# Optimization experiments

Hardware: AMD Instinct MI355X
Metric: run time of the kernel (lower is better)

## Reference

```python
import jax, jax.numpy as jnp
import numpy as np

N_SP, N_SPAT = 20000, 10000
E_SS, E_BIP, E_SP = 160000, 320000, 320000
H, C = 4, 64  # GAT heads / per-head channels (hidden_channels=64, concat=False)
EPS = 1e-6


def _gat(xs, xd, row, col, ea, Ws, Wd, a_s, a_d, a_e, We, b, num_dst, heads, ch, self_loops, concat):
    # PyG GATConv with edge_dim: linear -> per-head additive attention -> softmax over incoming edges -> scatter-add
    hs = (xs @ Ws).reshape(-1, heads, ch)          # [Ns,H,C]
    hd = (xd @ Wd).reshape(-1, heads, ch)          # [Nd,H,C]
    al_s = jnp.sum(hs * a_s, -1)                   # [Ns,H]
    al_d = jnp.sum(hd * a_d, -1)                   # [Nd,H]
    if self_loops:
        # add_self_loops with fill_value='mean': loop edge_attr = mean of incoming edge_attr per node
        cnt = jax.ops.segment_sum(jnp.ones((row.shape[0],), ea.dtype), col, num_dst)
        loop_ea = jax.ops.segment_sum(ea, col, num_dst) / jnp.maximum(cnt, 1.0)[:, None]
        loops = jnp.arange(num_dst, dtype=row.dtype)
        row = jnp.concatenate([row, loops])
        col = jnp.concatenate([col, loops])
        ea = jnp.concatenate([ea, loop_ea], 0)
    he = (ea @ We).reshape(-1, heads, ch)          # [E,H,C]
    al = jax.nn.leaky_relu(al_s[row] + al_d[col] + jnp.sum(he * a_e, -1), 0.2)  # [E,H]
    m = jax.ops.segment_max(al, col, num_segments=num_dst)
    ex = jnp.exp(al - m[col])
    den = jax.ops.segment_sum(ex, col, num_segments=num_dst)
    alpha = ex / (den[col] + 1e-16)
    out = jax.ops.segment_sum(hs[row] * alpha[..., None], col, num_segments=num_dst)  # [Nd,H,C]
    out = out.reshape(num_dst, heads * ch) if concat else out.mean(1)
    return out + b


def setup_inputs() -> dict:
    key = jax.random.key(0)
    ks = iter(jax.random.split(key, 64))
    f = lambda shape: jax.random.normal(next(ks), shape, jnp.float32)
    w = lambda shape: f(shape) / np.sqrt(shape[0])
    inp = {}
    inp['species_x_mean'] = f((N_SP, 32))
    inp['species_x_std'] = jax.random.uniform(next(ks), (N_SP, 32), jnp.float32)
    inp['traits_nanmask'] = jax.random.bernoulli(next(ks), 0.4, (N_SP, 32))
    inp['species_x_gen'] = f((N_SP, 64))
    inp['species_x_phylo'] = f((N_SP, 128))
    inp['spatial_x'] = f((N_SPAT, 12))
    inp['spatial_global_data'] = f((N_SPAT, 4))
    ei = lambda e, ns, nd: jnp.stack([jax.random.randint(next(ks), (e,), 0, ns, jnp.int32),
                                      jax.random.randint(next(ks), (e,), 0, nd, jnp.int32)])
    inp['ss_edge_index'] = ei(E_SS, N_SPAT, N_SPAT)
    inp['ss_edge_attr'] = jax.random.uniform(next(ks), (E_SS, 1), jnp.float32)
    inp['bip_edge_index'] = ei(E_BIP, N_SPAT, N_SP)
    inp['bip_edge_attr'] = jax.random.uniform(next(ks), (E_BIP, 1), jnp.float32)
    inp['sp_edge_index'] = ei(E_SP, N_SP, N_SP)
    inp['sp_edge_attr'] = jax.random.uniform(next(ks), (E_SP, 1), jnp.float32)
    # GAT conv params: space_gnn (sg0, sg1), species_gnn (pg0, pg1)
    for nm, din in [('sg0', 16), ('sg1', 64), ('pg0', 128), ('pg1', 64)]:
        inp[nm + '_W'] = w((din, H * C))
        inp[nm + '_as'] = f((H, C)) * 0.1
        inp[nm + '_ad'] = f((H, C)) * 0.1
        inp[nm + '_ae'] = f((H, C)) * 0.1
        inp[nm + '_We'] = w((1, H * C))
        inp[nm + '_b'] = jnp.zeros((C,), jnp.float32)
    # bipartite GATConv: heads=1, concat=True, src dim=hidden=64, dst dim=in_gen+in_phylo=192
    inp['bp_Ws'] = w((64, 64))
    inp['bp_Wd'] = w((192, 64))
    inp['bp_as'] = f((1, 64)) * 0.1
    inp['bp_ad'] = f((1, 64)) * 0.1
    inp['bp_ae'] = f((1, 64)) * 0.1
    inp['bp_We'] = w((1, 64))
    inp['bp_b'] = jnp.zeros((64,), jnp.float32)
    inp['sl_W'] = w((288, 64))
    inp['sl_b'] = jnp.zeros((64,), jnp.float32)
    inp['fc_W'] = w((64, 64))
    inp['fc_b'] = jnp.zeros((64,), jnp.float32)
    return inp


def reference(species_x_mean, species_x_std, traits_nanmask, species_x_gen, species_x_phylo,
              spatial_x, spatial_global_data, ss_edge_index, ss_edge_attr, bip_edge_index,
              bip_edge_attr, sp_edge_index, sp_edge_attr,
              sg0_W, sg0_as, sg0_ad, sg0_ae, sg0_We, sg0_b,
              sg1_W, sg1_as, sg1_ad, sg1_ae, sg1_We, sg1_b,
              pg0_W, pg0_as, pg0_ad, pg0_ae, pg0_We, pg0_b,
              pg1_W, pg1_as, pg1_ad, pg1_ae, pg1_We, pg1_b,
              bp_Ws, bp_Wd, bp_as, bp_ad, bp_ae, bp_We, bp_b,
              sl_W, sl_b, fc_W, fc_b):
    # inference path: no trait masking -> visibility = observed mask
    vis = (~traits_nanmask).astype(jnp.float32)
    sp_in = jnp.concatenate([species_x_mean, species_x_std, vis, species_x_gen, species_x_phylo], 1)
    sp_in = jax.nn.relu(sp_in @ sl_W + sl_b)                      # [N_SP,64]
    # spatial GNN (2 GATConv layers, heads=4, concat=False, self loops)
    h = jnp.concatenate([spatial_x, spatial_global_data], 1)      # [N_SPAT,16]
    r, c = ss_edge_index[0], ss_edge_index[1]
    h = jax.nn.relu(_gat(h, h, r, c, ss_edge_attr, sg0_W, sg0_W, sg0_as, sg0_ad, sg0_ae, sg0_We, sg0_b, N_SPAT, H, C, True, False))
    h = jax.nn.relu(_gat(h, h, r, c, ss_edge_attr, sg1_W, sg1_W, sg1_as, sg1_ad, sg1_ae, sg1_We, sg1_b, N_SPAT, H, C, True, False))
    # bipartite spatial->species GATConv (heads=1, concat=True, no self loops)
    part = jnp.concatenate([species_x_gen, species_x_phylo], 1)   # [N_SP,192]
    br, bc = bip_edge_index[0], bip_edge_index[1]
    sts = jax.nn.relu(_gat(h, part, br, bc, bip_edge_attr, bp_Ws, bp_Wd, bp_as, bp_ad, bp_ae, bp_We, bp_b, N_SP, 1, 64, False, True))
    # species GNN (2 GATConv layers)
    x = jnp.concatenate([sts, sp_in], 1)                          # [N_SP,128]
    pr, pc = sp_edge_index[0], sp_edge_index[1]
    x = jax.nn.relu(_gat(x, x, pr, pc, sp_edge_attr, pg0_W, pg0_W, pg0_as, pg0_ad, pg0_ae, pg0_We, pg0_b, N_SP, H, C, True, False))
    x = jax.nn.relu(_gat(x, x, pr, pc, sp_edge_attr, pg1_W, pg1_W, pg1_as, pg1_ad, pg1_ae, pg1_We, pg1_b, N_SP, H, C, True, False))
    ms = x @ fc_W + fc_b                                          # [N_SP, 2*out]
    mean, log_std = jnp.split(ms, 2, axis=-1)
    std = jax.nn.softplus(log_std) + EPS
    return mean, std
```

## Files before the change

### kernel.cpp

```cpp
#include <hip/hip_runtime.h>
#include <hip/hip_bf16.h>

#define NSP   20000
#define NSPAT 10000
#define ESS   160000
#define EBIP  320000
#define ESP   320000

static inline int cdiv_host(long a, long b) { return (int)((a + b - 1) / b); }

__device__ __forceinline__ float wave_red_sum(float p) {
#pragma unroll
  for (int m = 32; m >= 1; m >>= 1) p += __shfl_xor(p, m, 64);
  return p;
}
__device__ __forceinline__ float bf2f(unsigned short u) {
  return __uint_as_float(((unsigned int)u) << 16);
}
__device__ __forceinline__ unsigned short f2bf(float f) {
  unsigned int u = __float_as_uint(f);
  unsigned int r = (u + 0x7FFF + ((u >> 16) & 1)) >> 16;
  return (unsigned short)r;
}

// ... 220 lines not shown
  }

  float4 bv = make_float4(0.f, 0.f, 0.f, 0.f);
  float4 asv = make_float4(0.f, 0.f, 0.f, 0.f);
  float4 adv = make_float4(0.f, 0.f, 0.f, 0.f);
  if (J.bias) bv = *(const float4*)(J.bias + c0);
  if (J.a_s) asv = *(const float4*)(J.a_s + c0);
  if (J.a_d) adv = *(const float4*)(J.a_d + c0);

#pragma unroll
  for (int r = 0; r < 2; ++r) {
    long m = row0 + rg * 2 + r;
    bool ok = m < J.M;
    float v0 = acc[r][0] + bv.x, v1 = acc[r][1] + bv.y;
    float v2 = acc[r][2] + bv.z, v3 = acc[r][3] + bv.w;
    if (J.mode == 1) {
      if (ok)
        *(float4*)(J.Y + m * 64 + c0) = make_float4(
            fmaxf(v0, 0.f), fmaxf(v1, 0.f), fmaxf(v2, 0.f), fmaxf(v3, 0.f));
    } else if (J.mode == 2) {
      if (ok) {
        if (c0 < 32) {
          *(float4*)(J.Y + m * 32 + c0) = make_float4(v0, v1, v2, v3);
        } else {
          float4 o;
          o.x = fmaxf(v0, 0.f) + log1pf(__expf(-fabsf(v0))) + 1e-6f;
          o.y = fmaxf(v1, 0.f) + log1pf(__expf(-fabsf(v1))) + 1e-6f;
          o.z = fmaxf(v2, 0.f) + log1pf(__expf(-fabsf(v2))) + 1e-6f;
          o.w = fmaxf(v3, 0.f) + log1pf(__expf(-fabsf(v3))) + 1e-6f;
          *(float4*)(J.Y2 + m * 32 + (c0 - 32)) = o;
        }
      }
    } else if (ok && J.Y) {
      *(float4*)(J.Y + m * 64 + c0) = make_float4(v0, v1, v2, v3);
    }
    if (J.a_s) {
      float s = acc[r][0] * asv.x + acc[r][1] * asv.y + acc[r][2] * asv.z + acc[r][3] * asv.w;
      s += __shfl_xor(s, 1); s += __shfl_xor(s, 2);
      s += __shfl_xor(s, 4); s += __shfl_xor(s, 8);
      if (ok && cg == 0) J.al_s[m] = s;
    }
    if (J.a_d) {
      float s = acc[r][0] * adv.x + acc[r][1] * adv.y + acc[r][2] * adv.z + acc[r][3] * adv.w;
      s += __shfl_xor(s, 1); s += __shfl_xor(s, 2);
      s += __shfl_xor(s, 4); s += __shfl_xor(s, 8);
      if (ok && cg == 0) J.al_d[m] = s;
    }
  }
}

__global__ __launch_bounds__(256) void proj64x2l_kernel(PJob j0, PJob j1,
                                                        int nb0, int nb1,
                                                        LeafArgs la) {
  __shared__ float wl[32 * 64];
  __shared__ float xl[32 * 36];
  int b = blockIdx.x, t = threadIdx.x;
  if (b < nb0) {
    proj64_body(j0, b, wl, xl);
  } else if (b < nb0 + nb1) {
    proj64_body(j1, b - nb0, wl, xl);
  } else {
    int i = (b - nb0 - nb1) * 256 + t;
    if (i >= NSPAT + NSP) return;
    const int* ptr; const float* cea; float* lea; int d;
    if (i < NSPAT) { ptr = la.ss_ptr; cea = la.ss_cea; lea = la.ss_lea; d = i; }
    else { ptr = la.pp_ptr; cea = la.pp_cea; lea = la.pp_lea; d = i - NSPAT; }
    int e0 = ptr[d], e1 = ptr[d + 1];
    float s = 0.f;
    for (int e = e0; e < e1; ++e) s += cea[e];
    lea[d] = s / (float)max(e1 - e0, 1);
  }
}

__global__ __launch_bounds__(256) void proj_kernel(
    XSrc xsrc, int M, int K,
    const float* __restrict__ W,
    const float* __restrict__ a_s, const float* __restrict__ a_d,
    float* __restrict__ al_s, float* __restrict__ al_d,
    unsigned short* __restrict__ Y) {
  constexpr int KC = 32;
  constexpr int RPT = 8;
  constexpr int BR = 32;
  constexpr int KCP = 36;
  constexpr int H = 4;
  __shared__ float wl[KC * 256];
  __shared__ float xl[BR * KCP];

  int t = threadIdx.x;
  int cg = t & 63, rg = t >> 6;
  int c0 = cg * 4;
  long row0 = (long)blockIdx.x * BR;

  float acc[RPT][4];
#pragma unroll
  for (int r = 0; r < RPT; ++r)
#pragma unroll
    for (int j = 0; j < 4; ++j) acc[r][j] = 0.f;

  for (int k0 = 0; k0 < K; k0 += KC) {
    int kc = min(KC, K - k0);
    int seg = 0; int base = 0;
    while (k0 >= base + xsrc.w[seg]) { base += xsrc.w[seg]; ++seg; }
    const float* Xp = xsrc.p[seg];
    int stride = xsrc.w[seg];
    int kloc = k0 - base;

    __syncthreads();
    {
      const float4* wsrc = (const float4*)(W + (long)k0 * 256);
      float4* wdst = (float4*)wl;
      for (int i = t; i < (kc * 256) >> 2; i += 256) wdst[i] = wsrc[i];
    }
    for (int i = t; i < BR * 8; i += 256) {
      int r = i >> 3, kq = (i & 7) * 4;
      if (kq < kc) {
        long rr = row0 + r; if (rr >= M) rr = M - 1;
        float4 v = *(const float4*)(Xp + rr * stride + kloc + kq);
        *(float4*)(xl + r * KCP + kq) = v;
      }
    }
    __syncthreads();

    for (int kg = 0; kg < kc; kg += 4) {
      float4 w0 = *(const float4*)(wl + (kg + 0) * 256 + c0);
      float4 w1 = *(const float4*)(wl + (kg + 1) * 256 + c0);
      float4 w2 = *(const float4*)(wl + (kg + 2) * 256 + c0);
      float4 w3 = *(const float4*)(wl + (kg + 3) * 256 + c0);
      float4 xv[RPT];
#pragma unroll
      for (int r = 0; r < RPT; ++r)
        xv[r] = *(const float4*)(xl + (rg * RPT + r) * KCP + kg);
#pragma unroll
      for (int r = 0; r < RPT; ++r) {
        acc[r][0] = fmaf(xv[r].x, w0.x, acc[r][0]);
        acc[r][1] = fmaf(xv[r].x, w0.y, acc[r][1]);
        acc[r][2] = fmaf(xv[r].x, w0.z, acc[r][2]);
        acc[r][3] = fmaf(xv[r].x, w0.w, acc[r][3]);
        acc[r][0] = fmaf(xv[r].y, w1.x, acc[r][0]);
        acc[r][1] = fmaf(xv[r].y, w1.y, acc[r][1]);
        acc[r][2] = fmaf(xv[r].y, w1.z, acc[r][2]);
        acc[r][3] = fmaf(xv[r].y, w1.w, acc[r][3]);
        acc[r][0] = fmaf(xv[r].z, w2.x, acc[r][0]);
        acc[r][1] = fmaf(xv[r].z, w2.y, acc[r][1]);
        acc[r][2] = fmaf(xv[r].z, w2.z, acc[r][2]);
        acc[r][3] = fmaf(xv[r].z, w2.w, acc[r][3]);
        acc[r][0] = fmaf(xv[r].w, w3.x, acc[r][0]);
        acc[r][1] = fmaf(xv[r].w, w3.y, acc[r][1]);
        acc[r][2] = fmaf(xv[r].w, w3.z, acc[r][2]);
        acc[r][3] = fmaf(xv[r].w, w3.w, acc[r][3]);
      }
    }
  }

  float4 asv = *(const float4*)(a_s + c0);
  float4 adv = *(const float4*)(a_d + c0);

#pragma unroll
  for (int r = 0; r < RPT; ++r) {
    long m = row0 + (long)rg * RPT + r;
    bool ok = m < M;
    if (ok) {
      ushort4 o;
      o.x = f2bf(acc[r][0]); o.y = f2bf(acc[r][1]);
      o.z = f2bf(acc[r][2]); o.w = f2bf(acc[r][3]);
      *(ushort4*)(Y + m * 256 + c0) = o;
    }
    float s = acc[r][0] * asv.x + acc[r][1] * asv.y + acc[r][2] * asv.z + acc[r][3] * asv.w;
    s += __shfl_xor(s, 1); s += __shfl_xor(s, 2);
    s += __shfl_xor(s, 4); s += __shfl_xor(s, 8);
    if (ok && (cg & 15) == 0) al_s[m * H + (c0 >> 6)] = s;
    float d = acc[r][0] * adv.x + acc[r][1] * adv.y + acc[r][2] * adv.z + acc[r][3] * adv.w;
    d += __shfl_xor(d, 1); d += __shfl_xor(d, 2);
    d += __shfl_xor(d, 4); d += __shfl_xor(d, 8);
    if (ok && (cg & 15) == 0) al_d[m * H + (c0 >> 6)] = d;
  }
}

__device__ __forceinline__ void fma4_bf(float4& a, float al, ushort4 u) {
  a.x = fmaf(al, bf2f(u.x), a.x); a.y = fmaf(al, bf2f(u.y), a.y);
  a.z = fmaf(al, bf2f(u.z), a.z); a.w = fmaf(al, bf2f(u.w), a.w);
}
__device__ __forceinline__ void scale4(float4& a, float s) {
  a.x *= s; a.y *= s; a.z *= s; a.w *= s;
}

template <bool SELFLOOP>
__global__ __launch_bounds__(256) void gat4_fused(
    int Nd, const int* __restrict__ dptr, const int* __restrict__ csr_src,
    const float* __restrict__ csr_ea, const float* __restrict__ al_s,
    const float* __restrict__ al_d, const float* __restrict__ dote,
    const float* __restrict__ loop_ea, const unsigned short* __restrict__ hs,
    const float* __restrict__ bias, float* __restrict__ out) {
  int wave = threadIdx.x >> 6, lane = threadIdx.x & 63;
  int n = blockIdx.x * 4 + wave;
  if (n >= Nd) return;
  int h = lane >> 4;
  float ald = al_d[(long)n * 4 + h];
  float de = dote[h];
  int e0 = dptr[n], e1 = dptr[n + 1];
  float m0 = -INFINITY, d0 = 0.f;
  float4 a0 = make_float4(0.f, 0.f, 0.f, 0.f);
  if (SELFLOOP) {
    float l = al_s[(long)n * 4 + h] + ald + loop_ea[n] * de;
    l = (l > 0.f) ? l : 0.2f * l;
    m0 = l; d0 = 1.f;
    ushort4 u = *(const ushort4*)(hs + (long)n * 256 + lane * 4);
    a0.x = bf2f(u.x); a0.y = bf2f(u.y); a0.z = bf2f(u.z); a0.w = bf2f(u.w);
  }
  float m1 = -INFINITY, d1 = 0.f;
  float4 a1 = make_float4(0.f, 0.f, 0.f, 0.f);
  int e = e0;
  for (; e + 2 <= e1; e += 2) {
    int s0 = csr_src[e], s1 = csr_src[e + 1];
    float l0 = al_s[(long)s0 * 4 + h] + ald + csr_ea[e] * de;
    float l1 = al_s[(long)s1 * 4 + h] + ald + csr_ea[e + 1] * de;
    l0 = (l0 > 0.f) ? l0 : 0.2f * l0;
    l1 = (l1 > 0.f) ? l1 : 0.2f * l1;
    ushort4 u0 = *(const ushort4*)(hs + (long)s0 * 256 + lane * 4);
    ushort4 u1 = *(const ushort4*)(hs + (long)s1 * 256 + lane * 4);
    if (l0 > m0) { float sc = __expf(m0 - l0); d0 *= sc; scale4(a0, sc); m0 = l0; }
    float ex0 = __expf(l0 - m0);
    d0 += ex0;
    fma4_bf(a0, ex0, u0);
    if (l1 > m1) { float sc = __expf(m1 - l1); d1 *= sc; scale4(a1, sc); m1 = l1; }
    float ex1 = __expf(l1 - m1);
    d1 += ex1;
    fma4_bf(a1, ex1, u1);
  }
  if (e < e1) {
    int s0 = csr_src[e];
    float l0 = al_s[(long)s0 * 4 + h] + ald + csr_ea[e] * de;
    l0 = (l0 > 0.f) ? l0 : 0.2f * l0;
    ushort4 u0 = *(const ushort4*)(hs + (long)s0 * 256 + lane * 4);
    if (l0 > m0) { float sc = __expf(m0 - l0); d0 *= sc; scale4(a0, sc); m0 = l0; }
    float ex0 = __expf(l0 - m0);
    d0 += ex0;
    fma4_bf(a0, ex0, u0);
  }
  if (m1 != -INFINITY) {
    float M = fmaxf(m0, m1);
    float sA = (m0 == -INFINITY) ? 0.f : __expf(m0 - M);
    float sB = __expf(m1 - M);
    d0 = d0 * sA + d1 * sB;
    a0.x = a0.x * sA + a1.x * sB; a0.y = a0.y * sA + a1.y * sB;
    a0.z = a0.z * sA + a1.z * sB; a0.w = a0.w * sA + a1.w * sB;
  }
  float inv = 1.f / (d0 + 1e-16f);
  scale4(a0, inv);
  a0.x += __shfl_xor(a0.x, 16); a0.y += __shfl_xor(a0.y, 16);
  a0.z += __shfl_xor(a0.z, 16); a0.w += __shfl_xor(a0.w, 16);
  a0.x += __shfl_xor(a0.x, 32); a0.y += __shfl_xor(a0.y, 32);
  a0.z += __shfl_xor(a0.z, 32); a0.w += __shfl_xor(a0.w, 32);
  if (lane < 16) {
    float4 b = *(const float4*)(bias + lane * 4);
    float4 o;
    o.x = fmaxf(a0.x * 0.25f + b.x, 0.f);
    o.y = fmaxf(a0.y * 0.25f + b.y, 0.f);
    o.z = fmaxf(a0.z * 0.25f + b.z, 0.f);
    o.w = fmaxf(a0.w * 0.25f + b.w, 0.f);
    *(float4*)(out + (long)n * 64 + lane * 4) = o;
  }
}

__global__ __launch_bounds__(256) void gat1_fused(
    int Nd, const int* __restrict__ dptr, const int* __restrict__ csr_src,
    const float* __restrict__ csr_ea, const float* __restrict__ al_s,
    const float* __restrict__ al_d, const float* __restrict__ dote,
    const float* __restrict__ hs, const float* __restrict__ bias,
    float* __restrict__ out) {
  int wave = threadIdx.x >> 6, lane = threadIdx.x & 63;
  int n = blockIdx.x * 4 + wave;
  if (n >= Nd) return;
  float ald = al_d[n];
  float de = dote[0];
  int e0 = dptr[n], e1 = dptr[n + 1];
  float m0 = -INFINITY, d0 = 0.f, acc0 = 0.f;
  float m1 = -INFINITY, d1 = 0.f, acc1 = 0.f;
  int e = e0;
  for (; e + 2 <= e1; e += 2) {
    int s0 = csr_src[e], s1 = csr_src[e + 1];
    float l0 = al_s[s0] + ald + csr_ea[e] * de;
    float l1 = al_s[s1] + ald + csr_ea[e + 1] * de;
    l0 = (l0 > 0.f) ? l0 : 0.2f * l0;
    l1 = (l1 > 0.f) ? l1 : 0.2f * l1;
    float h0 = hs[(long)s0 * 64 + lane];
    float h1 = hs[(long)s1 * 64 + lane];
    if (l0 > m0) { float sc = __expf(m0 - l0); d0 *= sc; acc0 *= sc; m0 = l0; }
    float ex0 = __expf(l0 - m0);
    d0 += ex0; acc0 = fmaf(ex0, h0, acc0);
    if (l1 > m1) { float sc = __expf(m1 - l1); d1 *= sc; acc1 *= sc; m1 = l1; }
    float ex1 = __expf(l1 - m1);
    d1 += ex1; acc1 = fmaf(ex1, h1, acc1);
  }
  if (e < e1) {
    int s0 = csr_src[e];
    float l0 = al_s[s0] + ald + csr_ea[e] * de;
    l0 = (l0 > 0.f) ? l0 : 0.2f * l0;
    float h0 = hs[(long)s0 * 64 + lane];
    if (l0 > m0) { float sc = __expf(m0 - l0); d0 *= sc; acc0 *= sc; m0 = l0; }
    float ex0 = __expf(l0 - m0);
    d0 += ex0; acc0 = fmaf(ex0, h0, acc0);
  }
  if (m1 != -INFINITY) {
    float M = fmaxf(m0, m1);
    float sA = (m0 == -INFINITY) ? 0.f : __expf(m0 - M);
    float sB = __expf(m1 - M);
    d0 = d0 * sA + d1 * sB;
    acc0 = acc0 * sA + acc1 * sB;
  }
  float o = acc0 / (d0 + 1e-16f);
  out[(long)n * 64 + lane] = fmaxf(o + bias[lane], 0.f);
}

extern "C" void kernel_launch(void* const* d_in, const int* in_sizes, int n_in,
                              void* d_out, int out_size, void* d_ws, size_t ws_size,
                              hipStream_t stream) {
  const float* sp_mean = (const float*)d_in[0];
  const float* sp_std  = (const float*)d_in[1];
  const void*  nanmask = d_in[2];
  const float* sp_gen  = (const float*)d_in[3];
  const float* sp_phy  = (const float*)d_in[4];
  const float* spat_x  = (const float*)d_in[5];
  const float* spat_g  = (const float*)d_in[6];
  const int*   ss_ei   = (const int*)d_in[7];
  const float* ss_ea   = (const float*)d_in[8];
  const int*   bip_ei  = (const int*)d_in[9];
  const float* bip_ea  = (const float*)d_in[10];
  const int*   sp_ei   = (const int*)d_in[11];
  const float* sp_ea   = (const float*)d_in[12];
  const float* sg0_W = (const float*)d_in[13]; const float* sg0_as = (const float*)d_in[14];
  const float* sg0_ad = (const float*)d_in[15]; const float* sg0_ae = (const float*)d_in[16];
  const float* sg0_We = (const float*)d_in[17]; const float* sg0_b = (const float*)d_in[18];
  const float* sg1_W = (const float*)d_in[19]; const float* sg1_as = (const float*)d_in[20];
  const float* sg1_ad = (const float*)d_in[21]; const float* sg1_ae = (const float*)d_in[22];
  const float* sg1_We = (const float*)d_in[23]; const float* sg1_b = (const float*)d_in[24];
  const float* pg0_W = (const float*)d_in[25]; const float* pg0_as = (const float*)d_in[26];
  const float* pg0_ad = (const float*)d_in[27]; const float* pg0_ae = (const float*)d_in[28];
  const float* pg0_We = (const float*)d_in[29]; const float* pg0_b = (const float*)d_in[30];
  const float* pg1_W = (const float*)d_in[31]; const float* pg1_as = (const float*)d_in[32];
  const float* pg1_ad = (const float*)d_in[33]; const float* pg1_ae = (const float*)d_in[34];
  const float* pg1_We = (const float*)d_in[35]; const float* pg1_b = (const float*)d_in[36];
  const float* bp_Ws = (const float*)d_in[37]; const float* bp_Wd = (const float*)d_in[38];
  const float* bp_as = (const float*)d_in[39]; const float* bp_ad = (const float*)d_in[40];
  const float* bp_ae = (const float*)d_in[41]; const float* bp_We = (const float*)d_in[42];
  const float* bp_b  = (const float*)d_in[43];
  const float* sl_W  = (const float*)d_in[44]; const float* sl_b  = (const float*)d_in[45];
  const float* fc_W  = (const float*)d_in[46]; const float* fc_b  = (const float*)d_in[47];

  char* wsb = (char*)d_ws;
  size_t off = 0;
  auto A = [&](size_t nbytes) -> void* {
    void* p = wsb + off;
    off += (nbytes + 255) & ~(size_t)255;
    return p;
  };
  int* ss_cp = (int*)A((size_t)8 * NSPAT * 4);
  int* bp_cp = (int*)A((size_t)8 * NSP * 4);
  int* pp_cp = (int*)A((size_t)8 * NSP * 4);
  size_t zbytes = off;
  int*   ss_cnt = (int*)A((NSPAT + 1) * 4);
  int*   bp_cnt = (int*)A((NSP + 1) * 4);
  int*   pp_cnt = (int*)A((NSP + 1) * 4);
  int*   flag  = (int*)A(4);
  float* dotes = (float*)A(5 * 4 * sizeof(float));
  float* alS   = (float*)A((size_t)NSP * 4 * 4);
  float* alD   = (float*)A((size_t)NSP * 4 * 4);
  float* alSb  = (float*)A((size_t)NSPAT * 4);
  float* alDb  = (float*)A((size_t)NSP * 4);
  float* spc96 = (float*)A((size_t)NSP * 96 * 4);
  float* sp_in = (float*)A((size_t)NSP * 64 * 4);
  float* h0    = (float*)A((size_t)NSPAT * 16 * 4);
  float* h_a   = (float*)A((size_t)NSPAT * 64 * 4);
  float* h_b   = (float*)A((size_t)NSPAT * 64 * 4);
  float* HS    = (float*)A((size_t)NSP * 256 * 4);
  float* sts   = (float*)A((size_t)NSP * 64 * 4);
  float* x1    = (float*)A((size_t)NSP * 64 * 4);
  int*   ss_ptr = (int*)A((NSPAT + 1) * 4);
  int*   ss_src = (int*)A((size_t)ESS * 4);
  float* ss_cea = (float*)A((size_t)ESS * 4);
  int*   ss_rnk = (int*)A((size_t)ESS * 4);
  float* ss_lea = (float*)A((size_t)NSPAT * 4);
  int*   bp_ptr = (int*)A((NSP + 1) * 4);
  int*   bp_src = (int*)A((size_t)EBIP * 4);
  float* bp_cea = (float*)A((size_t)EBIP * 4);
  int*   bp_rnk = (int*)A((size_t)EBIP * 4);
  int*   pp_ptr = (int*)A((NSP + 1) * 4);
  int*   pp_src = (int*)A((size_t)ESP * 4);
  float* pp_cea = (float*)A((size_t)ESP * 4);
  int*   pp_rnk = (int*)A((size_t)ESP * 4);
  float* pp_lea = (float*)A((size_t)NSP * 4);
  (void)ws_size; (void)in_sizes; (void)n_in; (void)out_size;

  const int TB = 256;
  hipMemsetAsync(wsb, 0, zbytes, stream);

  count3_kernel<<<cdiv_host(ESS + EBIP + ESP, TB) + 1, TB, 0, stream>>>(
      ss_ei + ESS, ESS, ss_cp, ss_rnk, NSPAT,
      bip_ei + EBIP, EBIP, bp_cp, bp_rnk, NSP,
      sp_ei + ESP, ESP, pp_cp, pp_rnk, NSP,
      (const unsigned int*)nanmask, flag);
  merge3_kernel<<<cdiv_host(NSPAT + NSP + NSP, TB), TB, 0, stream>>>(
      ss_cp, ss_cnt, NSPAT, bp_cp, bp_cnt, NSP, pp_cp, pp_cnt, NSP);
  scan3_kernel<<<3, 1024, 0, stream>>>(ss_cnt, NSPAT, ss_ptr, bp_cnt, NSP, bp_ptr, pp_cnt, NSP, pp_ptr);

  {
    DoteArgs da{};
    da.We[0] = sg0_We; da.ae[0] = sg0_ae;
    da.We[1] = sg1_We; da.ae[1] = sg1_ae;
    da.We[2] = bp_We;  da.ae[2] = bp_ae;
    da.We[3] = pg0_We; da.ae[3] = pg0_ae;
    da.We[4] = pg1_We; da.ae[4] = pg1_ae;
    da.dotes = dotes;
    PrepArgs pa{ sp_mean, sp_std, nanmask, flag, spat_x, spat_g, spc96, h0 };
    int nb = cdiv_host(ESS + EBIP + ESP, TB) + 5 +
             cdiv_host((long)NSP * 96 + (long)NSPAT * 16, TB);
    scatter3x_kernel<<<nb, TB, 0, stream>>>(
        ss_ei, ss_ei + ESS, ss_ea, ESS, ss_ptr, ss_cp, ss_rnk, NSPAT, ss_src, ss_cea,
        bip_ei, bip_ei + EBIP, bip_ea, EBIP, bp_ptr, bp_cp, bp_rnk, NSP, bp_src, bp_cea,
        sp_ei, sp_ei + ESP, sp_ea, ESP, pp_ptr, pp_cp, pp_rnk, NSP, pp_src, pp_cea,
        da, pa);
  }

  {
    PJob j0{}; j0.xs.p[0] = spc96; j0.xs.w[0] = 96; j0.xs.p[1] = sp_gen; j0.xs.w[1] = 64;
    j0.xs.p[2] = sp_phy; j0.xs.w[2] = 128; j0.xs.n = 3;
    j0.M = NSP; j0.K = 288; j0.W = sl_W; j0.bias = sl_b; j0.mode = 1; j0.Y = sp_in;
    PJob j1{}; j1.xs.p[0] = sp_gen; j1.xs.w[0] = 64; j1.xs.p[1] = sp_phy; j1.xs.w[1] = 128;
    j1.xs.n = 2;
    j1.M = NSP; j1.K = 192; j1.W = bp_Wd; j1.mode = 0; j1.a_d = bp_ad; j1.al_d = alDb;
    LeafArgs la{ ss_ptr, ss_cea, ss_lea, pp_ptr, pp_cea, pp_lea };
    int nb0 = cdiv_host(NSP, 32), nb1 = cdiv_host(NSP, 32);
    int nbl = cdiv_host(NSPAT + NSP, TB);
    proj64x2l_kernel<<<nb0 + nb1 + nbl, TB, 0, stream>>>(j0, j1, nb0, nb1, la);
  }

  {
    XSrc xs{}; xs.p[0] = h0; xs.w[0] = 16; xs.n = 1;
    proj_kernel<<<cdiv_host(NSPAT, 32), TB, 0, stream>>>(xs, NSPAT, 16, sg0_W,
        sg0_as, sg0_ad, alS, alD, (unsigned short*)HS);
  }
  gat4_fused<true><<<cdiv_host(NSPAT, 4), TB, 0, stream>>>(
      NSPAT, ss_ptr, ss_src, ss_cea, alS, alD, dotes + 0, ss_lea,
      (const unsigned short*)HS, sg0_b, h_a);
  {
    XSrc xs{}; xs.p[0] = h_a; xs.w[0] = 64; xs.n = 1;
    proj_kernel<<<cdiv_host(NSPAT, 32), TB, 0, stream>>>(xs, NSPAT, 64, sg1_W,
        sg1_as, sg1_ad, alS, alD, (unsigned short*)HS);
  }
  gat4_fused<true><<<cdiv_host(NSPAT, 4), TB, 0, stream>>>(
      NSPAT, ss_ptr, ss_src, ss_cea, alS, alD, dotes + 4, ss_lea,
      (const unsigned short*)HS, sg1_b, h_b);

  {
    PJob j0{}; j0.xs.p[0] = h_b; j0.xs.w[0] = 64; j0.xs.n = 1;
    j0.M = NSPAT; j0.K = 64; j0.W = bp_Ws; j0.mode = 0;
    j0.a_s = bp_as; j0.al_s = alSb; j0.Y = h_a;
    LeafArgs la{ ss_ptr, ss_cea, ss_lea, pp_ptr, pp_cea, pp_lea };
    int nb0 = cdiv_host(NSPAT, 32);
    proj64x2l_kernel<<<nb0, TB, 0, stream>>>(j0, j0, nb0, 0, la);
  }
  gat1_fused<<<cdiv_host(NSP, 4), TB, 0, stream>>>(
      NSP, bp_ptr, bp_src, bp_cea, alSb, alDb, dotes + 8, h_a, bp_b, sts);

  {
    XSrc xs{}; xs.p[0] = sts; xs.w[0] = 64; xs.p[1] = sp_in; xs.w[1] = 64; xs.n = 2;
    proj_kernel<<<cdiv_host(NSP, 32), TB, 0, stream>>>(xs, NSP, 128, pg0_W,
        pg0_as, pg0_ad, alS, alD, (unsigned short*)HS);
  }
  gat4_fused<true><<<cdiv_host(NSP, 4), TB, 0, stream>>>(
      NSP, pp_ptr, pp_src, pp_cea, alS, alD, dotes + 12, pp_lea,
      (const unsigned short*)HS, pg0_b, x1);
  {
    XSrc xs{}; xs.p[0] = x1; xs.w[0] = 64; xs.n = 1;
    proj_kernel<<<cdiv_host(NSP, 32), TB, 0, stream>>>(xs, NSP, 64, pg1_W,
        pg1_as, pg1_ad, alS, alD, (unsigned short*)HS);
  }
  gat4_fused<true><<<cdiv_host(NSP, 4), TB, 0, stream>>>(
      NSP, pp_ptr, pp_src, pp_cea, alS, alD, dotes + 16, pp_lea,
      (const unsigned short*)HS, pg1_b, sts);

  {
    PJob j0{}; j0.xs.p[0] = sts; j0.xs.w[0] = 64; j0.xs.n = 1;
    j0.M = NSP; j0.K = 64; j0.W = fc_W; j0.bias = fc_b; j0.mode = 2;
    j0.Y = (float*)d_out; j0.Y2 = (float*)d_out + (long)NSP * 32;
    LeafArgs la{ ss_ptr, ss_cea, ss_lea, pp_ptr, pp_cea, pp_lea };
    int nb0 = cdiv_host(NSP, 32);
    proj64x2l_kernel<<<nb0, TB, 0, stream>>>(j0, j0, nb0, 0, la);
  }
}
```

Measured before the change: 497.0 us.

## Fuse GAT aggregation with the following projection through shared-memory tiles

Each GAT aggregation kernel now writes its 32-node output tile into shared memory, and the next layer's projection (256-wide or 64-wide, including the final FC/softplus head) runs in the same block from that tile. This removes the global-memory round trip of intermediate node features and cuts the launch count. Attention and feature buffers are double-buffered (A/B) so a layer can read the previous projection while writing the next. In exchange, each block now processes 8 nodes per wave sequentially, which gives fewer waves and less latency hiding in the gather phase, and it uses more LDS per block.

```diff
diff --git a/kernel.cpp b/kernel.cpp
--- a/kernel.cpp
+++ b/kernel.cpp
@@ -326,7 +326,6 @@
   constexpr int RPT = 8;
   constexpr int BR = 32;
   constexpr int KCP = 36;
-  constexpr int H = 4;
   __shared__ float wl[KC * 256];
   __shared__ float xl[BR * KCP];
 
@@ -412,11 +411,11 @@
     float s = acc[r][0] * asv.x + acc[r][1] * asv.y + acc[r][2] * asv.z + acc[r][3] * asv.w;
     s += __shfl_xor(s, 1); s += __shfl_xor(s, 2);
     s += __shfl_xor(s, 4); s += __shfl_xor(s, 8);
-    if (ok && (cg & 15) == 0) al_s[m * H + (c0 >> 6)] = s;
+    if (ok && (cg & 15) == 0) al_s[m * 4 + (c0 >> 6)] = s;
     float d = acc[r][0] * adv.x + acc[r][1] * adv.y + acc[r][2] * adv.z + acc[r][3] * adv.w;
     d += __shfl_xor(d, 1); d += __shfl_xor(d, 2);
     d += __shfl_xor(d, 4); d += __shfl_xor(d, 8);
-    if (ok && (cg & 15) == 0) al_d[m * H + (c0 >> 6)] = d;
+    if (ok && (cg & 15) == 0) al_d[m * 4 + (c0 >> 6)] = d;
   }
 }
 
@@ -428,132 +427,348 @@
   a.x *= s; a.y *= s; a.z *= s; a.w *= s;
 }
 
-template <bool SELFLOOP>
-__global__ __launch_bounds__(256) void gat4_fused(
-    int Nd, const int* __restrict__ dptr, const int* __restrict__ csr_src,
-    const float* __restrict__ csr_ea, const float* __restrict__ al_s,
-    const float* __restrict__ al_d, const float* __restrict__ dote,
-    const float* __restrict__ loop_ea, const unsigned short* __restrict__ hs,
-    const float* __restrict__ bias, float* __restrict__ out) {
+struct G4A {
+  int Nd;
+  const int* dptr; const int* src; const float* cea;
+  const float* al_s; const float* al_d; const float* dote;
+  const float* lea; const unsigned short* hs; const float* bias;
+};
+struct G1A {
+  int Nd;
+  const int* dptr; const int* src; const float* cea;
+  const float* al_s; const float* al_d; const float* dote;
+  const float* hs; const float* bias;
+};
+struct PF256 {
+  int M, K;
+  const float* W; const float* xg;
+  const float* a_s; const float* a_d;
+  float* al_s; float* al_d;
+  unsigned short* Y;
+};
+struct PF64 {
+  int M;
+  const float* W; const float* bias; int mode;
+  const float* a_s; float* al_s;
+  float* Y; float* Y2;
+};
+
+__device__ void gat4_phase(const G4A& g, int b, float* hbuf) {
   int wave = threadIdx.x >> 6, lane = threadIdx.x & 63;
-  int n = blockIdx.x * 4 + wave;
-  if (n >= Nd) return;
   int h = lane >> 4;
-  float ald = al_d[(long)n * 4 + h];
-  float de = dote[h];
-  int e0 = dptr[n], e1 = dptr[n + 1];
-  float m0 = -INFINITY, d0 = 0.f;
-  float4 a0 = make_float4(0.f, 0.f, 0.f, 0.f);
-  if (SELFLOOP) {
-    float l = al_s[(long)n * 4 + h] + ald + loop_ea[n] * de;
+  float de = g.dote[h];
+  for (int i = 0; i < 8; ++i) {
+    int ln = wave * 8 + i;
+    int n = b * 32 + ln;
+    if (n >= g.Nd) continue;
+    float ald = g.al_d[(long)n * 4 + h];
+    int e0 = g.dptr[n], e1 = g.dptr[n + 1];
+    float l = g.al_s[(long)n * 4 + h] + ald + g.lea[n] * de;
     l = (l > 0.f) ? l : 0.2f * l;
-    m0 = l; d0 = 1.f;
-    ushort4 u = *(const ushort4*)(hs + (long)n * 256 + lane * 4);
-    a0.x = bf2f(u.x); a0.y = bf2f(u.y); a0.z = bf2f(u.z); a0.w = bf2f(u.w);
-  }
-  float m1 = -INFINITY, d1 = 0.f;
-  float4 a1 = make_float4(0.f, 0.f, 0.f, 0.f);
-  int e = e0;
-  for (; e + 2 <= e1; e += 2) {
-    int s0 = csr_src[e], s1 = csr_src[e + 1];
-    float l0 = al_s[(long)s0 * 4 + h] + ald + csr_ea[e] * de;
-    float l1 = al_s[(long)s1 * 4 + h] + ald + csr_ea[e + 1] * de;
-    l0 = (l0 > 0.f) ? l0 : 0.2f * l0;
-    l1 = (l1 > 0.f) ? l1 : 0.2f * l1;
-    ushort4 u0 = *(const ushort4*)(hs + (long)s0 * 256 + lane * 4);
-    ushort4 u1 = *(const ushort4*)(hs + (long)s1 * 256 + lane * 4);
-    if (l0 > m0) { float sc = __expf(m0 - l0); d0 *= sc; scale4(a0, sc); m0 = l0; }
-    float ex0 = __expf(l0 - m0);
-    d0 += ex0;
-    fma4_bf(a0, ex0, u0);
-    if (l1 > m1) { float sc = __expf(m1 - l1); d1 *= sc; scale4(a1, sc); m1 = l1; }
-    float ex1 = __expf(l1 - m1);
-    d1 += ex1;
-    fma4_bf(a1, ex1, u1);
-  }
-  if (e < e1) {
-    int s0 = csr_src[e];
-    float l0 = al_s[(long)s0 * 4 + h] + ald + csr_ea[e] * de;
-    l0 = (l0 > 0.f) ? l0 : 0.2f * l0;
-    ushort4 u0 = *(const ushort4*)(hs + (long)s0 * 256 + lane * 4);
-    if (l0 > m0) { float sc = __expf(m0 - l0); d0 *= sc; scale4(a0, sc); m0 = l0; }
-    float ex0 = __expf(l0 - m0);
-    d0 += ex0;
-    fma4_bf(a0, ex0, u0);
-  }
-  if (m1 != -INFINITY) {
-    float M = fmaxf(m0, m1);
-    float sA = (m0 == -INFINITY) ? 0.f : __expf(m0 - M);
-    float sB = __expf(m1 - M);
-    d0 = d0 * sA + d1 * sB;
-    a0.x = a0.x * sA + a1.x * sB; a0.y = a0.y * sA + a1.y * sB;
-    a0.z = a0.z * sA + a1.z * sB; a0.w = a0.w * sA + a1.w * sB;
-  }
-  float inv = 1.f / (d0 + 1e-16f);
-  scale4(a0, inv);
-  a0.x += __shfl_xor(a0.x, 16); a0.y += __shfl_xor(a0.y, 16);
-  a0.z += __shfl_xor(a0.z, 16); a0.w += __shfl_xor(a0.w, 16);
-  a0.x += __shfl_xor(a0.x, 32); a0.y += __shfl_xor(a0.y, 32);
-  a0.z += __shfl_xor(a0.z, 32); a0.w += __shfl_xor(a0.w, 32);
-  if (lane < 16) {
-    float4 b = *(const float4*)(bias + lane * 4);
-    float4 o;
-    o.x = fmaxf(a0.x * 0.25f + b.x, 0.f);
-    o.y = fmaxf(a0.y * 0.25f + b.y, 0.f);
-    o.z = fmaxf(a0.z * 0.25f + b.z, 0.f);
-    o.w = fmaxf(a0.w * 0.25f + b.w, 0.f);
-    *(float4*)(out + (long)n * 64 + lane * 4) = o;
-  }
-}
-
-__global__ __launch_bounds__(256) void gat1_fused(
-    int Nd, const int* __restrict__ dptr, const int* __restrict__ csr_src,
-    const float* __restrict__ csr_ea, const float* __restrict__ al_s,
-    const float* __restrict__ al_d, const float* __restrict__ dote,
-    const float* __restrict__ hs, const float* __restrict__ bias,
-    float* __restrict__ out) {
+    float m0 = l, d0 = 1.f;
+    float4 a0;
+    {
+      ushort4 u = *(const ushort4*)(g.hs + (long)n * 256 + lane * 4);
+      a0.x = bf2f(u.x); a0.y = bf2f(u.y); a0.z = bf2f(u.z); a0.w = bf2f(u.w);
+    }
+    float m1 = -INFINITY, d1 = 0.f;
+    float4 a1 = make_float4(0.f, 0.f, 0.f, 0.f);
+    int e = e0;
+    for (; e + 2 <= e1; e += 2) {
+      int s0 = g.src[e], s1 = g.src[e + 1];
+      float l0 = g.al_s[(long)s0 * 4 + h] + ald + g.cea[e] * de;
+      float l1 = g.al_s[(long)s1 * 4 + h] + ald + g.cea[e + 1] * de;
+      l0 = (l0 > 0.f) ? l0 : 0.2f * l0;
+      l1 = (l1 > 0.f) ? l1 : 0.2f * l1;
+      ushort4 u0 = *(const ushort4*)(g.hs + (long)s0 * 256 + lane * 4);
+      ushort4 u1 = *(const ushort4*)(g.hs + (long)s1 * 256 + lane * 4);
+      if (l0 > m0) { float sc = __expf(m0 - l0); d0 *= sc; scale4(a0, sc); m0 = l0; }
+      float ex0 = __expf(l0 - m0);
+      d0 += ex0;
+      fma4_bf(a0, ex0, u0);
+      if (l1 > m1) { float sc = __expf(m1 - l1); d1 *= sc; scale4(a1, sc); m1 = l1; }
+      float ex1 = __expf(l1 - m1);
+      d1 += ex1;
+      fma4_bf(a1, ex1, u1);
+    }
+    if (e < e1) {
+      int s0 = g.src[e];
+      float l0 = g.al_s[(long)s0 * 4 + h] + ald + g.cea[e] * de;
+      l0 = (l0 > 0.f) ? l0 : 0.2f * l0;
+      ushort4 u0 = *(const ushort4*)(g.hs + (long)s0 * 256 + lane * 4);
+      if (l0 > m0) { float sc = __expf(m0 - l0); d0 *= sc; scale4(a0, sc); m0 = l0; }
+      float ex0 = __expf(l0 - m0);
+      d0 += ex0;
+      fma4_bf(a0, ex0, u0);
+    }
+    if (m1 != -INFINITY) {
+      float M = fmaxf(m0, m1);
+      float sA = __expf(m0 - M);
+      float sB = __expf(m1 - M);
+      d0 = d0 * sA + d1 * sB;
+      a0.x = a0.x * sA + a1.x * sB; a0.y = a0.y * sA + a1.y * sB;
+      a0.z = a0.z * sA + a1.z * sB; a0.w = a0.w * sA + a1.w * sB;
+    }
+    float inv = 1.f / (d0 + 1e-16f);
+    scale4(a0, inv);
+    a0.x += __shfl_xor(a0.x, 16); a0.y += __shfl_xor(a0.y, 16);
+    a0.z += __shfl_xor(a0.z, 16); a0.w += __shfl_xor(a0.w, 16);
+    a0.x += __shfl_xor(a0.x, 32); a0.y += __shfl_xor(a0.y, 32);
+    a0.z += __shfl_xor(a0.z, 32); a0.w += __shfl_xor(a0.w, 32);
+    if (lane < 16) {
+      float4 bv = *(const float4*)(g.bias + lane * 4);
+      float4 o;
+      o.x = fmaxf(a0.x * 0.25f + bv.x, 0.f);
+      o.y = fmaxf(a0.y * 0.25f + bv.y, 0.f);
+      o.z = fmaxf(a0.z * 0.25f + bv.z, 0.f);
+      o.w = fmaxf(a0.w * 0.25f + bv.w, 0.f);
+      *(float4*)(hbuf + ln * 64 + lane * 4) = o;
+    }
+  }
+}
+
+__device__ void gat1_phase(const G1A& g, int b, float* hbuf) {
   int wave = threadIdx.x >> 6, lane = threadIdx.x & 63;
-  int n = blockIdx.x * 4 + wave;
-  if (n >= Nd) return;
-  float ald = al_d[n];
-  float de = dote[0];
-  int e0 = dptr[n], e1 = dptr[n + 1];
-  float m0 = -INFINITY, d0 = 0.f, acc0 = 0.f;
-  float m1 = -INFINITY, d1 = 0.f, acc1 = 0.f;
-  int e = e0;
-  for (; e + 2 <= e1; e += 2) {
-    int s0 = csr_src[e], s1 = csr_src[e + 1];
-    float l0 = al_s[s0] + ald + csr_ea[e] * de;
-    float l1 = al_s[s1] + ald + csr_ea[e + 1] * de;
-    l0 = (l0 > 0.f) ? l0 : 0.2f * l0;
-    l1 = (l1 > 0.f) ? l1 : 0.2f * l1;
-    float h0 = hs[(long)s0 * 64 + lane];
-    float h1 = hs[(long)s1 * 64 + lane];
-    if (l0 > m0) { float sc = __expf(m0 - l0); d0 *= sc; acc0 *= sc; m0 = l0; }
-    float ex0 = __expf(l0 - m0);
-    d0 += ex0; acc0 = fmaf(ex0, h0, acc0);
-    if (l1 > m1) { float sc = __expf(m1 - l1); d1 *= sc; acc1 *= sc; m1 = l1; }
-    float ex1 = __expf(l1 - m1);
-    d1 += ex1; acc1 = fmaf(ex1, h1, acc1);
-  }
-  if (e < e1) {
-    int s0 = csr_src[e];
-    float l0 = al_s[s0] + ald + csr_ea[e] * de;
-    l0 = (l0 > 0.f) ? l0 : 0.2f * l0;
-    float h0 = hs[(long)s0 * 64 + lane];
-    if (l0 > m0) { float sc = __expf(m0 - l0); d0 *= sc; acc0 *= sc; m0 = l0; }
-    float ex0 = __expf(l0 - m0);
-    d0 += ex0; acc0 = fmaf(ex0, h0, acc0);
-  }
-  if (m1 != -INFINITY) {
-    float M = fmaxf(m0, m1);
-    float sA = (m0 == -INFINITY) ? 0.f : __expf(m0 - M);
-    float sB = __expf(m1 - M);
-    d0 = d0 * sA + d1 * sB;
-    acc0 = acc0 * sA + acc1 * sB;
-  }
-  float o = acc0 / (d0 + 1e-16f);
-  out[(long)n * 64 + lane] = fmaxf(o + bias[lane], 0.f);
+  float de = g.dote[0];
+  for (int i = 0; i < 8; ++i) {
+    int ln = wave * 8 + i;
+    int n = b * 32 + ln;
+    if (n >= g.Nd) continue;
+    float ald = g.al_d[n];
+    int e0 = g.dptr[n], e1 = g.dptr[n + 1];
+    float m0 = -INFINITY, d0 = 0.f, acc0 = 0.f;
+    float m1 = -INFINITY, d1 = 0.f, acc1 = 0.f;
+    int e = e0;
+    for (; e + 2 <= e1; e += 2) {
+      int s0 = g.src[e], s1 = g.src[e + 1];
+      float l0 = g.al_s[s0] + ald + g.cea[e] * de;
+      float l1 = g.al_s[s1] + ald + g.cea[e + 1] * de;
+      l0 = (l0 > 0.f) ? l0 : 0.2f * l0;
+      l1 = (l1 > 0.f) ? l1 : 0.2f * l1;
+      float h0 = g.hs[(long)s0 * 64 + lane];
+      float h1 = g.hs[(long)s1 * 64 + lane];
+      if (l0 > m0) { float sc = __expf(m0 - l0); d0 *= sc; acc0 *= sc; m0 = l0; }
+      float ex0 = __expf(l0 - m0);
+      d0 += ex0; acc0 = fmaf(ex0, h0, acc0);
+      if (l1 > m1) { float sc = __expf(m1 - l1); d1 *= sc; acc1 *= sc; m1 = l1; }
+      float ex1 = __expf(l1 - m1);
+      d1 += ex1; acc1 = fmaf(ex1, h1, acc1);
+    }
+    if (e < e1) {
+      int s0 = g.src[e];
+      float l0 = g.al_s[s0] + ald + g.cea[e] * de;
+      l0 = (l0 > 0.f) ? l0 : 0.2f * l0;
+      float h0 = g.hs[(long)s0 * 64 + lane];
+      if (l0 > m0) { float sc = __expf(m0 - l0); d0 *= sc; acc0 *= sc; m0 = l0; }
+      float ex0 = __expf(l0 - m0);
+      d0 += ex0; acc0 = fmaf(ex0, h0, acc0);
+    }
+    if (m1 != -INFINITY) {
+      float M = fmaxf(m0, m1);
+      float sA = (m0 == -INFINITY) ? 0.f : __expf(m0 - M);
+      float sB = __expf(m1 - M);
+      d0 = d0 * sA + d1 * sB;
+      acc0 = acc0 * sA + acc1 * sB;
+    }
+    float o = acc0 / (d0 + 1e-16f);
+    hbuf[ln * 64 + lane] = fmaxf(o + g.bias[lane], 0.f);
+  }
+}
+
+__device__ void proj256_fused(const PF256& p, int b, const float* hbuf,
+                              float* wl, float* xl) {
+  constexpr int KC = 32, RPT = 8, KCP = 36;
+  int t = threadIdx.x;
+  int cg = t & 63, rg = t >> 6;
+  int c0 = cg * 4;
+  long row0 = (long)b * 32;
+
+  float acc[RPT][4];
+#pragma unroll
+  for (int r = 0; r < RPT; ++r)
+#pragma unroll
+    for (int j = 0; j < 4; ++j) acc[r][j] = 0.f;
+
+  for (int k0 = 0; k0 < p.K; k0 += KC) {
+    bool fromLds = (k0 < 64);
+    __syncthreads();
+    {
+      const float4* wsrc = (const float4*)(p.W + (long)k0 * 256);
+      float4* wdst = (float4*)wl;
+      for (int i = t; i < (KC * 256) >> 2; i += 256) wdst[i] = wsrc[i];
+    }
+    if (!fromLds) {
+      int r = t >> 3, kq = (t & 7) * 4;
+      long rr = row0 + r; if (rr >= p.M) rr = p.M - 1;
+      float4 v = *(const float4*)(p.xg + rr * 64 + (k0 - 64) + kq);
+      *(float4*)(xl + r * KCP + kq) = v;
+    }
+    __syncthreads();
+
+    for (int kg = 0; kg < KC; kg += 4) {
+      float4 w0 = *(const float4*)(wl + (kg + 0) * 256 + c0);
+      float4 w1 = *(const float4*)(wl + (kg + 1) * 256 + c0);
+      float4 w2 = *(const float4*)(wl + (kg + 2) * 256 + c0);
+      float4 w3 = *(const float4*)(wl + (kg + 3) * 256 + c0);
+      float4 xv[RPT];
+#pragma unroll
+      for (int r = 0; r < RPT; ++r)
+        xv[r] = fromLds ? *(const float4*)(hbuf + (rg * RPT + r) * 64 + k0 + kg)
+                        : *(const float4*)(xl + (rg * RPT + r) * KCP + kg);
+#pragma unroll
+      for (int r = 0; r < RPT; ++r) {
+        acc[r][0] = fmaf(xv[r].x, w0.x, acc[r][0]);
+        acc[r][1] = fmaf(xv[r].x, w0.y, acc[r][1]);
+        acc[r][2] = fmaf(xv[r].x, w0.z, acc[r][2]);
+        acc[r][3] = fmaf(xv[r].x, w0.w, acc[r][3]);
+        acc[r][0] = fmaf(xv[r].y, w1.x, acc[r][0]);
+        acc[r][1] = fmaf(xv[r].y, w1.y, acc[r][1]);
+        acc[r][2] = fmaf(xv[r].y, w1.z, acc[r][2]);
+        acc[r][3] = fmaf(xv[r].y, w1.w, acc[r][3]);
+        acc[r][0] = fmaf(xv[r].z, w2.x, acc[r][0]);
+        acc[r][1] = fmaf(xv[r].z, w2.y, acc[r][1]);
+        acc[r][2] = fmaf(xv[r].z, w2.z, acc[r][2]);
+        acc[r][3] = fmaf(xv[r].z, w2.w, acc[r][3]);
+        acc[r][0] = fmaf(xv[r].w, w3.x, acc[r][0]);
+        acc[r][1] = fmaf(xv[r].w, w3.y, acc[r][1]);
+        acc[r][2] = fmaf(xv[r].w, w3.z, acc[r][2]);
+        acc[r][3] = fmaf(xv[r].w, w3.w, acc[r][3]);
+      }
+    }
+  }
+
+  float4 asv = *(const float4*)(p.a_s + c0);
+  float4 adv = *(const float4*)(p.a_d + c0);
+#pragma unroll
+  for (int r = 0; r < RPT; ++r) {
+    long m = row0 + (long)rg * RPT + r;
+    bool ok = m < p.M;
+    if (ok) {
+      ushort4 o;
+      o.x = f2bf(acc[r][0]); o.y = f2bf(acc[r][1]);
+      o.z = f2bf(acc[r][2]); o.w = f2bf(acc[r][3]);
+      *(ushort4*)(p.Y + m * 256 + c0) = o;
+    }
+    float s = acc[r][0] * asv.x + acc[r][1] * asv.y + acc[r][2] * asv.z + acc[r][3] * asv.w;
+    s += __shfl_xor(s, 1); s += __shfl_xor(s, 2);
+    s += __shfl_xor(s, 4); s += __shfl_xor(s, 8);
+    if (ok && (cg & 15) == 0) p.al_s[m * 4 + (c0 >> 6)] = s;
+    float d = acc[r][0] * adv.x + acc[r][1] * adv.y + acc[r][2] * adv.z + acc[r][3] * adv.w;
+    d += __shfl_xor(d, 1); d += __shfl_xor(d, 2);
+    d += __shfl_xor(d, 4); d += __shfl_xor(d, 8);
+    if (ok && (cg & 15) == 0) p.al_d[m * 4 + (c0 >> 6)] = d;
+  }
+}
+
+__device__ void proj64_fused(const PF64& p, int b, const float* hbuf, float* wl) {
+  int t = threadIdx.x;
+  int cg = t & 15, rg = t >> 4;
+  int c0 = cg * 4;
+  long row0 = (long)b * 32;
+
+  float acc[2][4];
+#pragma unroll
+  for (int r = 0; r < 2; ++r)
+#pragma unroll
+    for (int j = 0; j < 4; ++j) acc[r][j] = 0.f;
+
+  for (int k0 = 0; k0 < 64; k0 += 32) {
+    __syncthreads();
+    {
+      const float4* ws = (const float4*)(p.W + (long)k0 * 64);
+      float4* wd = (float4*)wl;
+      wd[t] = ws[t];
+      wd[t + 256] = ws[t + 256];
+    }
+    __syncthreads();
+    for (int kg = 0; kg < 32; kg += 4) {
+      float4 w0 = *(const float4*)(wl + (kg + 0) * 64 + c0);
+      float4 w1 = *(const float4*)(wl + (kg + 1) * 64 + c0);
+      float4 w2 = *(const float4*)(wl + (kg + 2) * 64 + c0);
+      float4 w3 = *(const float4*)(wl + (kg + 3) * 64 + c0);
+#pragma unroll
+      for (int r = 0; r < 2; ++r) {
+        float4 xv = *(const float4*)(hbuf + (rg * 2 + r) * 64 + k0 + kg);
+        acc[r][0] = fmaf(xv.x, w0.x, acc[r][0]);
+        acc[r][1] = fmaf(xv.x, w0.y, acc[r][1]);
+        acc[r][2] = fmaf(xv.x, w0.z, acc[r][2]);
+        acc[r][3] = fmaf(xv.x, w0.w, acc[r][3]);
+        acc[r][0] = fmaf(xv.y, w1.x, acc[r][0]);
+        acc[r][1] = fmaf(xv.y, w1.y, acc[r][1]);
+        acc[r][2] = fmaf(xv.y, w1.z, acc[r][2]);
+        acc[r][3] = fmaf(xv.y, w1.w, acc[r][3]);
+        acc[r][0] = fmaf(xv.z, w2.x, acc[r][0]);
+        acc[r][1] = fmaf(xv.z, w2.y, acc[r][1]);
+        acc[r][2] = fmaf(xv.z, w2.z, acc[r][2]);
+        acc[r][3] = fmaf(xv.z, w2.w, acc[r][3]);
+        acc[r][0] = fmaf(xv.w, w3.x, acc[r][0]);
+        acc[r][1] = fmaf(xv.w, w3.y, acc[r][1]);
+        acc[r][2] = fmaf(xv.w, w3.z, acc[r][2]);
+        acc[r][3] = fmaf(xv.w, w3.w, acc[r][3]);
+      }
+    }
+  }
+
+  float4 bv = make_float4(0.f, 0.f, 0.f, 0.f);
+  float4 asv = make_float4(0.f, 0.f, 0.f, 0.f);
+  if (p.bias) bv = *(const float4*)(p.bias + c0);
+  if (p.a_s) asv = *(const float4*)(p.a_s + c0);
+
+#pragma unroll
+  for (int r = 0; r < 2; ++r) {
+    long m = row0 + rg * 2 + r;
+    bool ok = m < p.M;
+    float v0 = acc[r][0] + bv.x, v1 = acc[r][1] + bv.y;
+    float v2 = acc[r][2] + bv.z, v3 = acc[r][3] + bv.w;
+    if (p.mode == 2) {
+      if (ok) {
+        if (c0 < 32) {
+          *(float4*)(p.Y + m * 32 + c0) = make_float4(v0, v1, v2, v3);
+        } else {
+          float4 o;
+          o.x = fmaxf(v0, 0.f) + log1pf(__expf(-fabsf(v0))) + 1e-6f;
+          o.y = fmaxf(v1, 0.f) + log1pf(__expf(-fabsf(v1))) + 1e-6f;
+          o.z = fmaxf(v2, 0.f) + log1pf(__expf(-fabsf(v2))) + 1e-6f;
+          o.w = fmaxf(v3, 0.f) + log1pf(__expf(-fabsf(v3))) + 1e-6f;
+          *(float4*)(p.Y2 + m * 32 + (c0 - 32)) = o;
+        }
+      }
+    } else if (ok && p.Y) {
+      *(float4*)(p.Y + m * 64 + c0) = make_float4(v0, v1, v2, v3);
+    }
+    if (p.a_s) {
+      float s = acc[r][0] * asv.x + acc[r][1] * asv.y + acc[r][2] * asv.z + acc[r][3] * asv.w;
+      s += __shfl_xor(s, 1); s += __shfl_xor(s, 2);
+      s += __shfl_xor(s, 4); s += __shfl_xor(s, 8);
+      if (ok && cg == 0) p.al_s[m] = s;
+    }
+  }
+}
+
+__global__ __launch_bounds__(256) void g4p256_kernel(G4A g, PF256 p) {
+  __shared__ __align__(16) float wl[32 * 256];
+  __shared__ __align__(16) float xl[32 * 36];
+  __shared__ __align__(16) float hbuf[32 * 64];
+  gat4_phase(g, blockIdx.x, hbuf);
+  __syncthreads();
+  proj256_fused(p, blockIdx.x, hbuf, wl, xl);
+}
+
+__global__ __launch_bounds__(256) void g1p256_kernel(G1A g, PF256 p) {
+  __shared__ __align__(16) float wl[32 * 256];
+  __shared__ __align__(16) float xl[32 * 36];
+  __shared__ __align__(16) float hbuf[32 * 64];
+  gat1_phase(g, blockIdx.x, hbuf);
+  __syncthreads();
+  proj256_fused(p, blockIdx.x, hbuf, wl, xl);
+}
+
+__global__ __launch_bounds__(256) void g4p64_kernel(G4A g, PF64 p) {
+  __shared__ __align__(16) float wl[32 * 64];
+  __shared__ __align__(16) float hbuf[32 * 64];
+  gat4_phase(g, blockIdx.x, hbuf);
+  __syncthreads();
+  proj64_fused(p, blockIdx.x, hbuf, wl);
 }
 
 extern "C" void kernel_launch(void* const* d_in, const int* in_sizes, int n_in,
@@ -607,18 +822,18 @@
   int*   pp_cnt = (int*)A((NSP + 1) * 4);
   int*   flag  = (int*)A(4);
   float* dotes = (float*)A(5 * 4 * sizeof(float));
-  float* alS   = (float*)A((size_t)NSP * 4 * 4);
-  float* alD   = (float*)A((size_t)NSP * 4 * 4);
+  float* alS_A = (float*)A((size_t)NSP * 4 * 4);
+  float* alD_A = (float*)A((size_t)NSP * 4 * 4);
+  float* alS_B = (float*)A((size_t)NSP * 4 * 4);
+  float* alD_B = (float*)A((size_t)NSP * 4 * 4);
   float* alSb  = (float*)A((size_t)NSPAT * 4);
   float* alDb  = (float*)A((size_t)NSP * 4);
   float* spc96 = (float*)A((size_t)NSP * 96 * 4);
   float* sp_in = (float*)A((size_t)NSP * 64 * 4);
   float* h0    = (float*)A((size_t)NSPAT * 16 * 4);
-  float* h_a   = (float*)A((size_t)NSPAT * 64 * 4);
-  float* h_b   = (float*)A((size_t)NSPAT * 64 * 4);
-  float* HS    = (float*)A((size_t)NSP * 256 * 4);
-  float* sts   = (float*)A((size_t)NSP * 64 * 4);
-  float* x1    = (float*)A((size_t)NSP * 64 * 4);
+  float* h_src = (float*)A((size_t)NSPAT * 64 * 4);
+  unsigned short* HS_A = (unsigned short*)A((size_t)NSP * 256 * 2);
+  unsigned short* HS_B = (unsigned short*)A((size_t)NSP * 256 * 2);
   int*   ss_ptr = (int*)A((NSPAT + 1) * 4);
   int*   ss_src = (int*)A((size_t)ESS * 4);
   float* ss_cea = (float*)A((size_t)ESS * 4);
@@ -681,54 +896,37 @@
   {
     XSrc xs{}; xs.p[0] = h0; xs.w[0] = 16; xs.n = 1;
     proj_kernel<<<cdiv_host(NSPAT, 32), TB, 0, stream>>>(xs, NSPAT, 16, sg0_W,
-        sg0_as, sg0_ad, alS, alD, (unsigned short*)HS);
-  }
-  gat4_fused<true><<<cdiv_host(NSPAT, 4), TB, 0, stream>>>(
-      NSPAT, ss_ptr, ss_src, ss_cea, alS, alD, dotes + 0, ss_lea,
-      (const unsigned short*)HS, sg0_b, h_a);
+        sg0_as, sg0_ad, alS_A, alD_A, HS_A);
+  }
+
   {
-    XSrc xs{}; xs.p[0] = h_a; xs.w[0] = 64; xs.n = 1;
-    proj_kernel<<<cdiv_host(NSPAT, 32), TB, 0, stream>>>(xs, NSPAT, 64, sg1_W,
-        sg1_as, sg1_ad, alS, alD, (unsigned short*)HS);
-  }
-  gat4_fused<true><<<cdiv_host(NSPAT, 4), TB, 0, stream>>>(
-      NSPAT, ss_ptr, ss_src, ss_cea, alS, alD, dotes + 4, ss_lea,
-      (const unsigned short*)HS, sg1_b, h_b);
+    G4A g{ NSPAT, ss_ptr, ss_src, ss_cea, alS_A, alD_A, dotes + 0, ss_lea, HS_A, sg0_b };
+    PF256 p{ NSPAT, 64, sg1_W, nullptr, sg1_as, sg1_ad, alS_B, alD_B, HS_B };
+    g4p256_kernel<<<cdiv_host(NSPAT, 32), TB, 0, stream>>>(g, p);
+  }
 
   {
-    PJob j0{}; j0.xs.p[0] = h_b; j0.xs.w[0] = 64; j0.xs.n = 1;
-    j0.M = NSPAT; j0.K = 64; j0.W = bp_Ws; j0.mode = 0;
-    j0.a_s = bp_as; j0.al_s = alSb; j0.Y = h_a;
-    LeafArgs la{ ss_ptr, ss_cea, ss_lea, pp_ptr, pp_cea, pp_lea };
-    int nb0 = cdiv_host(NSPAT, 32);
-    proj64x2l_kernel<<<nb0, TB, 0, stream>>>(j0, j0, nb0, 0, la);
-  }
-  gat1_fused<<<cdiv_host(NSP, 4), TB, 0, stream>>>(
-      NSP, bp_ptr, bp_src, bp_cea, alSb, alDb, dotes + 8, h_a, bp_b, sts);
+    G4A g{ NSPAT, ss_ptr, ss_src, ss_cea, alS_B, alD_B, dotes + 4, ss_lea, HS_B, sg1_b };
+    PF64 p{ NSPAT, bp_Ws, nullptr, 0, bp_as, alSb, h_src, nullptr };
+    g4p64_kernel<<<cdiv_host(NSPAT, 32), TB, 0, stream>>>(g, p);
+  }
 
   {
-    XSrc xs{}; xs.p[0] = sts; xs.w[0] = 64; xs.p[1] = sp_in; xs.w[1] = 64; xs.n = 2;
-    proj_kernel<<<cdiv_host(NSP, 32), TB, 0, stream>>>(xs, NSP, 128, pg0_W,
-        pg0_as, pg0_ad, alS, alD, (unsigned short*)HS);
-  }
-  gat4_fused<true><<<cdiv_host(NSP, 4), TB, 0, stream>>>(
-      NSP, pp_ptr, pp_src, pp_cea, alS, alD, dotes + 12, pp_lea,
-      (const unsigned short*)HS, pg0_b, x1);
+    G1A g{ NSP, bp_ptr, bp_src, bp_cea, alSb, alDb, dotes + 8, h_src, bp_b };
+    PF256 p{ NSP, 128, pg0_W, sp_in, pg0_as, pg0_ad, alS_A, alD_A, HS_A };
+    g1p256_kernel<<<cdiv_host(NSP, 32), TB, 0, stream>>>(g, p);
+  }
+
   {
-    XSrc xs{}; xs.p[0] = x1; xs.w[0] = 64; xs.n = 1;
-    proj_kernel<<<cdiv_host(NSP, 32), TB, 0, stream>>>(xs, NSP, 64, pg1_W,
-        pg1_as, pg1_ad, alS, alD, (unsigned short*)HS);
-  }
-  gat4_fused<true><<<cdiv_host(NSP, 4), TB, 0, stream>>>(
-      NSP, pp_ptr, pp_src, pp_cea, alS, alD, dotes + 16, pp_lea,
-      (const unsigned short*)HS, pg1_b, sts);
+    G4A g{ NSP, pp_ptr, pp_src, pp_cea, alS_A, alD_A, dotes + 12, pp_lea, HS_A, pg0_b };
+    PF256 p{ NSP, 64, pg1_W, nullptr, pg1_as, pg1_ad, alS_B, alD_B, HS_B };
+    g4p256_kernel<<<cdiv_host(NSP, 32), TB, 0, stream>>>(g, p);
+  }
 
   {
-    PJob j0{}; j0.xs.p[0] = sts; j0.xs.w[0] = 64; j0.xs.n = 1;
-    j0.M = NSP; j0.K = 64; j0.W = fc_W; j0.bias = fc_b; j0.mode = 2;
-    j0.Y = (float*)d_out; j0.Y2 = (float*)d_out + (long)NSP * 32;
-    LeafArgs la{ ss_ptr, ss_cea, ss_lea, pp_ptr, pp_cea, pp_lea };
-    int nb0 = cdiv_host(NSP, 32);
-    proj64x2l_kernel<<<nb0, TB, 0, stream>>>(j0, j0, nb0, 0, la);
-  }
-}
+    G4A g{ NSP, pp_ptr, pp_src, pp_cea, alS_B, alD_B, dotes + 16, pp_lea, HS_B, pg1_b };
+    PF64 p{ NSP, fc_W, fc_b, 2, nullptr, nullptr,
+            (float*)d_out, (float*)d_out + (long)NSP * 32 };
+    g4p64_kernel<<<cdiv_host(NSP, 32), TB, 0, stream>>>(g, p);
+  }
+}
```

After: 740.9 us. 1.49x slower.
